# Performance work log

Measured on AMD Instinct MI355X. Metric: run time of the kernel, lower is better.

The kernel has to match this reference:

```python
import jax, jax.numpy as jnp
import numpy as np

PAD_VALUE = 0.0


def setup_inputs() -> dict:
    key = jax.random.key(0)
    k1, k2 = jax.random.split(key)
    B, DIM, T = 16, 384, 512
    x = jax.random.normal(k1, (B, DIM, T), dtype=jnp.float32)
    duration = jax.random.randint(k2, (B, T), 0, 8, dtype=jnp.int32)
    return {"x": x, "duration": duration, "d_max": T * 8}


def reference(x, duration, d_max):
    """Length regulator (FastSpeech-style).

    x:        (B, dim, T) float32
    duration: (B, T) int32, frames per input timestep
    d_max:    static int, padded output frame length (>= max total duration)

    Returns:
      out:     (B, dim, d_max) expanded/padded tensor
      mel_len: (B,) int32 true output lengths
    """
    B, dim, T = x.shape
    # Guard against all-zero duration rows (original fills them with 1s).
    row_sum = duration.sum(axis=1)  # (B,)
    duration = jnp.where((row_sum == 0)[:, None], jnp.ones_like(duration), duration)

    cum = jnp.cumsum(duration, axis=1)  # (B, T) exclusive-end offsets
    mel_len = cum[:, -1]  # (B,)

    frames = jnp.arange(d_max, dtype=jnp.int32)  # (d_max,)
    # Source index for each output frame: first t with cum[t] > frame.
    idx = jax.vmap(lambda c: jnp.searchsorted(c, frames, side="right"))(cum)  # (B, d_max)
    idx = jnp.clip(idx, 0, T - 1)

    out = jnp.take_along_axis(x, idx[:, None, :], axis=2)  # (B, dim, d_max)
    valid = frames[None, :] < mel_len[:, None]  # (B, d_max)
    out = jnp.where(valid[:, None, :], out, jnp.asarray(PAD_VALUE, x.dtype))
    return out, mel_len
```

## Files before the change

kernel.cpp:

```cpp
#include <hip/hip_runtime.h>

#define B_SZ   16
#define DIM_SZ 384
#define T_SZ   512
#define DMAX   4096
#define DC     8
#define FC     2048

__global__ __launch_bounds__(64) void lr_scan_kernel(const int* __restrict__ duration,
                                                     int* __restrict__ ws_cum,
                                                     int* __restrict__ ws_mel,
                                                     float* __restrict__ mel_out) {
    const int b = blockIdx.x;
    const int l = threadIdx.x;
    const int4* __restrict__ src = (const int4*)(duration + b * T_SZ);
    const int4 a = src[l * 2];
    const int4 c = src[l * 2 + 1];
    int p[8];
    p[0] = a.x;        p[1] = p[0] + a.y; p[2] = p[1] + a.z; p[3] = p[2] + a.w;
    p[4] = p[3] + c.x; p[5] = p[4] + c.y; p[6] = p[5] + c.z; p[7] = p[6] + c.w;
    int s = p[7];
#pragma unroll
    for (int off = 1; off < 64; off <<= 1) {
        const int v = __shfl_up(s, off);
        if (l >= off) s += v;
    }
    const int excl   = s - p[7];
    const int rowsum = __shfl(s, 63);
    int4 o0, o1;
    if (rowsum == 0) {
        const int t0 = l * 8;
        o0 = make_int4(t0 + 1, t0 + 2, t0 + 3, t0 + 4);
        o1 = make_int4(t0 + 5, t0 + 6, t0 + 7, t0 + 8);
    } else {
        o0 = make_int4(excl + p[0], excl + p[1], excl + p[2], excl + p[3]);
        o1 = make_int4(excl + p[4], excl + p[5], excl + p[6], excl + p[7]);
    }
    int4* __restrict__ dst = (int4*)(ws_cum + b * T_SZ);
    dst[l * 2]     = o0;
    dst[l * 2 + 1] = o1;
    if (l == 63) {
        const int ml = (rowsum == 0) ? T_SZ : rowsum;
        ws_mel[b] = ml;
        mel_out[b] = (float)ml;
    }
}

__global__ __launch_bounds__(256) void lr_gather_kernel(const float* __restrict__ x,
                                                        const int* __restrict__ ws_cum,
                                                        const int* __restrict__ ws_mel,
                                                        float* __restrict__ out) {
    __shared__ float s_x[DC * T_SZ];
    __shared__ int   s_cum[T_SZ];
    const int tid = threadIdx.x;
    const int b   = blockIdx.y;
    const int d0  = blockIdx.z * DC;
    const int f0  = blockIdx.x * FC;

    s_cum[tid]       = ws_cum[b * T_SZ + tid];
    s_cum[tid + 256] = ws_cum[b * T_SZ + tid + 256];

    const float4* __restrict__ xsrc = (const float4*)(x + ((size_t)b * DIM_SZ + d0) * T_SZ);
    float4* s_x4 = (float4*)s_x;
#pragma unroll
    for (int i = 0; i < (DC * T_SZ / 4) / 256; ++i)
        s_x4[i * 256 + tid] = xsrc[i * 256 + tid];
    __syncthreads();

    const int mel = ws_mel[b];
    float4* __restrict__ outp = (float4*)(out + (size_t)b * DIM_SZ * DMAX);

#pragma unroll
    for (int g = 0; g < FC / 1024; ++g) {
        const int f  = f0 + g * 1024 + tid * 4;
        const int f4 = f >> 2;
        if (f >= mel) {
            const float4 z = make_float4(0.f, 0.f, 0.f, 0.f);
#pragma unroll
            for (int dd = 0; dd < DC; ++dd)
                outp[(size_t)(d0 + dd) * (DMAX / 4) + f4] = z;
        } else {
            int  idx[4];
            bool valid[4];
#pragma unroll
            for (int j = 0; j < 4; ++j) {
                const int ff = f + j;
                int pos = 0;
#pragma unroll
                for (int step = 256; step > 0; step >>= 1) {
                    if (s_cum[pos + step - 1] <= ff) pos += step;
                }
                idx[j]   = pos;
                valid[j] = (ff < mel);
            }
#pragma unroll
            for (int dd = 0; dd < DC; ++dd) {
                const float* __restrict__ xr = s_x + dd * T_SZ;
                float4 v;
                v.x = valid[0] ? xr[idx[0]] : 0.0f;
                v.y = valid[1] ? xr[idx[1]] : 0.0f;
                v.z = valid[2] ? xr[idx[2]] : 0.0f;
                v.w = valid[3] ? xr[idx[3]] : 0.0f;
                outp[(size_t)(d0 + dd) * (DMAX / 4) + f4] = v;
            }
        }
    }
}

extern "C" void kernel_launch(void* const* d_in, const int* in_sizes, int n_in,
                              void* d_out, int out_size, void* d_ws, size_t ws_size,
                              hipStream_t stream) {
    const float* x        = (const float*)d_in[0];
    const int*   duration = (const int*)d_in[1];

    float* out     = (float*)d_out;
    float* mel_out = out + (size_t)B_SZ * DIM_SZ * DMAX;

    int* ws_cum = (int*)d_ws;
    int* ws_mel = ws_cum + B_SZ * T_SZ;

    lr_scan_kernel<<<B_SZ, 64, 0, stream>>>(duration, ws_cum, ws_mel, mel_out);

    dim3 grid(DMAX / FC, B_SZ, DIM_SZ / DC);
    lr_gather_kernel<<<grid, 256, 0, stream>>>(x, ws_cum, ws_mel, out);
}
```

Baseline: 116.4 us.

## Fuse duration scan into gather kernel with nontemporal stores and early zero-fill

Removes the separate scan kernel, so each gather block recomputes the cumulative durations for its batch row in shared memory. This drops a launch and the global workspace round-trip. The tiling changes to 4 channels by the full frame range per block, and the padding zeros are written before the x tile is staged to overlap latency. All output stores become nontemporal. In exchange, the scan is redundantly recomputed by every block.

```diff
diff --git a/kernel.cpp b/kernel.cpp
--- a/kernel.cpp
+++ b/kernel.cpp
@@ -4,82 +4,85 @@
 #define DIM_SZ 384
 #define T_SZ   512
 #define DMAX   4096
-#define DC     8
-#define FC     2048
+#define DC     4
 
-__global__ __launch_bounds__(64) void lr_scan_kernel(const int* __restrict__ duration,
-                                                     int* __restrict__ ws_cum,
-                                                     int* __restrict__ ws_mel,
-                                                     float* __restrict__ mel_out) {
-    const int b = blockIdx.x;
-    const int l = threadIdx.x;
-    const int4* __restrict__ src = (const int4*)(duration + b * T_SZ);
-    const int4 a = src[l * 2];
-    const int4 c = src[l * 2 + 1];
-    int p[8];
-    p[0] = a.x;        p[1] = p[0] + a.y; p[2] = p[1] + a.z; p[3] = p[2] + a.w;
-    p[4] = p[3] + c.x; p[5] = p[4] + c.y; p[6] = p[5] + c.z; p[7] = p[6] + c.w;
-    int s = p[7];
-#pragma unroll
-    for (int off = 1; off < 64; off <<= 1) {
-        const int v = __shfl_up(s, off);
-        if (l >= off) s += v;
-    }
-    const int excl   = s - p[7];
-    const int rowsum = __shfl(s, 63);
-    int4 o0, o1;
-    if (rowsum == 0) {
-        const int t0 = l * 8;
-        o0 = make_int4(t0 + 1, t0 + 2, t0 + 3, t0 + 4);
-        o1 = make_int4(t0 + 5, t0 + 6, t0 + 7, t0 + 8);
-    } else {
-        o0 = make_int4(excl + p[0], excl + p[1], excl + p[2], excl + p[3]);
-        o1 = make_int4(excl + p[4], excl + p[5], excl + p[6], excl + p[7]);
-    }
-    int4* __restrict__ dst = (int4*)(ws_cum + b * T_SZ);
-    dst[l * 2]     = o0;
-    dst[l * 2 + 1] = o1;
-    if (l == 63) {
-        const int ml = (rowsum == 0) ? T_SZ : rowsum;
-        ws_mel[b] = ml;
-        mel_out[b] = (float)ml;
-    }
-}
+typedef float f4 __attribute__((ext_vector_type(4)));
 
-__global__ __launch_bounds__(256) void lr_gather_kernel(const float* __restrict__ x,
-                                                        const int* __restrict__ ws_cum,
-                                                        const int* __restrict__ ws_mel,
-                                                        float* __restrict__ out) {
+__global__ __launch_bounds__(256) void lr_fused_kernel(const float* __restrict__ x,
+                                                       const int* __restrict__ duration,
+                                                       float* __restrict__ out,
+                                                       float* __restrict__ mel_out) {
     __shared__ float s_x[DC * T_SZ];
     __shared__ int   s_cum[T_SZ];
+    __shared__ int   s_mel;
     const int tid = threadIdx.x;
     const int b   = blockIdx.y;
-    const int d0  = blockIdx.z * DC;
-    const int f0  = blockIdx.x * FC;
+    const int d0  = blockIdx.x * DC;
 
-    s_cum[tid]       = ws_cum[b * T_SZ + tid];
-    s_cum[tid + 256] = ws_cum[b * T_SZ + tid + 256];
+    const f4* __restrict__ xsrc = (const f4*)(x + ((size_t)b * DIM_SZ + d0) * T_SZ);
+    const f4 r0 = xsrc[tid];
+    const f4 r1 = xsrc[tid + 256];
 
-    const float4* __restrict__ xsrc = (const float4*)(x + ((size_t)b * DIM_SZ + d0) * T_SZ);
-    float4* s_x4 = (float4*)s_x;
+    if (tid < 64) {
+        const int4* __restrict__ dsrc = (const int4*)(duration + b * T_SZ);
+        const int4 a = dsrc[tid * 2];
+        const int4 c = dsrc[tid * 2 + 1];
+        int p0 = a.x,      p1 = p0 + a.y, p2 = p1 + a.z, p3 = p2 + a.w;
+        int p4 = p3 + c.x, p5 = p4 + c.y, p6 = p5 + c.z, p7 = p6 + c.w;
+        int s = p7;
 #pragma unroll
-    for (int i = 0; i < (DC * T_SZ / 4) / 256; ++i)
-        s_x4[i * 256 + tid] = xsrc[i * 256 + tid];
+        for (int off = 1; off < 64; off <<= 1) {
+            const int v = __shfl_up(s, off);
+            if (tid >= off) s += v;
+        }
+        const int excl   = s - p7;
+        const int rowsum = __shfl(s, 63);
+        int4 o0, o1;
+        if (rowsum == 0) {
+            const int t0 = tid * 8;
+            o0 = make_int4(t0 + 1, t0 + 2, t0 + 3, t0 + 4);
+            o1 = make_int4(t0 + 5, t0 + 6, t0 + 7, t0 + 8);
+        } else {
+            o0 = make_int4(excl + p0, excl + p1, excl + p2, excl + p3);
+            o1 = make_int4(excl + p4, excl + p5, excl + p6, excl + p7);
+        }
+        int4* cdst = (int4*)s_cum;
+        cdst[tid * 2]     = o0;
+        cdst[tid * 2 + 1] = o1;
+        if (tid == 63) {
+            const int ml = (rowsum == 0) ? T_SZ : rowsum;
+            s_mel = ml;
+            if (blockIdx.x == 0) mel_out[b] = (float)ml;
+        }
+    }
     __syncthreads();
 
-    const int mel = ws_mel[b];
-    float4* __restrict__ outp = (float4*)(out + (size_t)b * DIM_SZ * DMAX);
+    const int mel = s_mel;
+    f4* __restrict__ outp = (f4*)(out + (size_t)b * DIM_SZ * DMAX);
+    const f4 z = {0.f, 0.f, 0.f, 0.f};
+
+    bool need[4];
+#pragma unroll
+    for (int g = 0; g < 4; ++g) {
+        const int f = g * 1024 + tid * 4;
+        need[g] = (f < mel);
+        if (!need[g]) {
+            const int f4i = (f >> 2);
+#pragma unroll
+            for (int dd = 0; dd < DC; ++dd)
+                __builtin_nontemporal_store(z, &outp[(size_t)(d0 + dd) * (DMAX / 4) + f4i]);
+        }
+    }
+
+    f4* s_x4 = (f4*)s_x;
+    s_x4[tid]       = r0;
+    s_x4[tid + 256] = r1;
+    __syncthreads();
 
 #pragma unroll
-    for (int g = 0; g < FC / 1024; ++g) {
-        const int f  = f0 + g * 1024 + tid * 4;
-        const int f4 = f >> 2;
-        if (f >= mel) {
-            const float4 z = make_float4(0.f, 0.f, 0.f, 0.f);
-#pragma unroll
-            for (int dd = 0; dd < DC; ++dd)
-                outp[(size_t)(d0 + dd) * (DMAX / 4) + f4] = z;
-        } else {
+    for (int g = 0; g < 4; ++g) {
+        if (need[g]) {
+            const int f = g * 1024 + tid * 4;
             int  idx[4];
             bool valid[4];
 #pragma unroll
@@ -93,15 +96,16 @@
                 idx[j]   = pos;
                 valid[j] = (ff < mel);
             }
+            const int f4i = (f >> 2);
 #pragma unroll
             for (int dd = 0; dd < DC; ++dd) {
                 const float* __restrict__ xr = s_x + dd * T_SZ;
-                float4 v;
+                f4 v;
                 v.x = valid[0] ? xr[idx[0]] : 0.0f;
                 v.y = valid[1] ? xr[idx[1]] : 0.0f;
                 v.z = valid[2] ? xr[idx[2]] : 0.0f;
                 v.w = valid[3] ? xr[idx[3]] : 0.0f;
-                outp[(size_t)(d0 + dd) * (DMAX / 4) + f4] = v;
+                __builtin_nontemporal_store(v, &outp[(size_t)(d0 + dd) * (DMAX / 4) + f4i]);
             }
         }
     }
@@ -116,11 +120,6 @@
     float* out     = (float*)d_out;
     float* mel_out = out + (size_t)B_SZ * DIM_SZ * DMAX;
 
-    int* ws_cum = (int*)d_ws;
-    int* ws_mel = ws_cum + B_SZ * T_SZ;
-
-    lr_scan_kernel<<<B_SZ, 64, 0, stream>>>(duration, ws_cum, ws_mel, mel_out);
-
-    dim3 grid(DMAX / FC, B_SZ, DIM_SZ / DC);
-    lr_gather_kernel<<<grid, 256, 0, stream>>>(x, ws_cum, ws_mel, out);
+    dim3 grid(DIM_SZ / DC, B_SZ);
+    lr_fused_kernel<<<grid, 256, 0, stream>>>(x, duration, out, mel_out);
 }
```

Measured after the change: 117.8 us. No clear change (+1.1%).
